# Kernel optimization log

Hardware: AMD Instinct MI355X
Metric: run time of the kernel (lower is better)

## Reference

```python
import jax, jax.numpy as jnp
import numpy as np

B, S, E, HD = 32, 1024, 768, 64
NUM_IMAGE_PATCHES = 49


def setup_inputs() -> dict:
    key = jax.random.key(0)
    ks = jax.random.split(key, 9)
    w = 0.02
    return {
        "decoder_sequence": jax.random.normal(ks[0], (B, S, E), dtype=jnp.float32),
        "Wq": jax.random.normal(ks[1], (E, HD), dtype=jnp.float32) * w,
        "bq": jnp.zeros((HD,), dtype=jnp.float32),
        "Wk": jax.random.normal(ks[2], (E, HD), dtype=jnp.float32) * w,
        "bk": jnp.zeros((HD,), dtype=jnp.float32),
        "Wv": jax.random.normal(ks[3], (E, HD), dtype=jnp.float32) * w,
        "bv": jnp.zeros((HD,), dtype=jnp.float32),
        "input_sequence_length": 975,
        "padding_mask": jax.random.randint(ks[4], (B, 1, S), 0, 2).astype(bool),
    }


def reference(decoder_sequence, Wq, bq, Wk, bk, Wv, bv, input_sequence_length, padding_mask):
    # single-head projections: [B,S,E] @ [E,HD] -> [B,S,HD]
    Q = decoder_sequence @ Wq + bq
    K = decoder_sequence @ Wk + bk
    V = decoder_sequence @ Wv + bv

    scores = jnp.einsum('bid,bjd->bij', Q, K) / jnp.sqrt(jnp.float32(HD))

    # mask: image-patch rows (i < 49) fully unmasked; text region is causal
    # (mask[49:,49:] = triu(-inf, diag=1)), i.e. -inf where i >= 49 and j > i.
    i = jnp.arange(S)[:, None]
    j = jnp.arange(S)[None, :]
    causal_bad = (i >= NUM_IMAGE_PATCHES) & (j > i)  # [S,S]
    scores = jnp.where(causal_bad[None, :, :], -jnp.inf, scores)

    # padding mask on keys, broadcast over queries: [B,1,S] -> [B,S,S]
    scores = jnp.where(padding_mask, -jnp.inf, scores)

    A = jax.nn.softmax(scores, axis=-1)
    H = jnp.einsum('bij,bjd->bid', A, V)
    return H
```

## Files before the change

### kernel.cpp

```cpp
#include <hip/hip_runtime.h>
#include <stdint.h>
#include <stddef.h>


typedef __attribute__((ext_vector_type(8))) short bf16x8;
typedef __attribute__((ext_vector_type(4))) float f32x4;

#define NIP 49
#define QSCALE 0.18033688011112042f

#define GLDS16(g, l)                                      \
  __builtin_amdgcn_global_load_lds(                       \
      (const __attribute__((address_space(1))) void*)(g), \
      (__attribute__((address_space(3))) void*)(l), 16, 0, 0)

__device__ __forceinline__ short f2b(float f) {
  union { float f; uint32_t u; } c; c.f = f;
  uint32_t u = c.u;
  uint32_t r = (u + 0x7fffu + ((u >> 16) & 1u)) >> 16;
  return (short)(uint16_t)r;
}

__global__ __launch_bounds__(256) void wt_kernel(
    const float* __restrict__ Wq, const float* __restrict__ Wk,
    const float* __restrict__ Wv, short* __restrict__ Wt) {
  int idx = blockIdx.x * 256 + threadIdx.x;
  int n = idx / 768;
  int k = idx - n * 768;
  const float* W = (n < 64) ? Wq : (n < 128) ? Wk : Wv;
  Wt[idx] = f2b(W[(size_t)k * 64 + (n & 63)]);
}

__global__ __launch_bounds__(256, 2) void proj_kernel(
    const float* __restrict__ X, const float* __restrict__ bq,
    const float* __restrict__ bk, const float* __restrict__ bv,
    const short* __restrict__ Wt, short* __restrict__ Qg,
    short* __restrict__ Kg, short* __restrict__ Vt) {
  __shared__ short lX[2][2][64][32];
  __shared__ short lW[2][2][192][32];
  const int tid = threadIdx.x;
  const int wid = tid >> 6, lane = tid & 63;
  const int l15 = lane & 15, q4 = lane >> 4;
  const int r0 = blockIdx.x * 64;

  float4 rx[4];
  auto xload = [&](int kb) {
#pragma unroll
    for (int i = 0; i < 4; ++i) {
      const int xi = tid + i * 256;
      rx[i] = *(const float4*)(X + (size_t)(r0 + (xi >> 4)) * 768 + kb + (xi & 15) * 4);
    }
  };
  auto xstage = [&](int buf) {
#pragma unroll
    for (int i = 0; i < 4; ++i) {
      const int xi = tid + i * 256;
      short4 s;
      s.x = f2b(rx[i].x); s.y = f2b(rx[i].y); s.z = f2b(rx[i].z); s.w = f2b(rx[i].w);
      *(short4*)&lX[buf][(xi & 15) >> 3][xi >> 4][(xi & 7) * 4] = s;
    }
  };
  const int wr = lane >> 2, wc = (lane & 3) * 8;
  auto wlds = [&](int buf, int kb) {
#pragma unroll
    for (int i = 0; i < 6; ++i) {
      const int fi = wid * 6 + i;
      const int j = fi >> 1, ks = fi & 1;
      GLDS16(Wt + (size_t)(j * 16 + wr) * 768 + kb + ks * 32 + wc,
             &lW[buf][ks][j * 16][0]);
    }
  };

  f32x4 acc[12];
#pragma unroll
  for (int c = 0; c < 12; ++c) acc[c] = (f32x4){0.f, 0.f, 0.f, 0.f};

  xload(0);
  wlds(0, 0);
  xstage(0);
  __syncthreads();

#pragma unroll
  for (int st = 0; st < 12; ++st) {
    const int cur = st & 1;
    if (st + 1 < 12) {
      xload((st + 1) * 64);
      wlds(cur ^ 1, (st + 1) * 64);
    }
#pragma unroll
    for (int ks = 0; ks < 2; ++ks) {
      bf16x8 a = *(const bf16x8*)&lX[cur][ks][wid * 16 + l15][q4 * 8];
#pragma unroll
      for (int c = 0; c < 12; ++c) {
        bf16x8 bw = *(const bf16x8*)&lW[cur][ks][c * 16 + l15][q4 * 8];
        acc[c] = __builtin_amdgcn_mfma_f32_16x16x32_bf16(a, bw, acc[c], 0, 0, 0);
      }
    }
    if (st + 1 < 12) xstage(cur ^ 1);
    __syncthreads();
  }

  const int b = r0 >> 10, s0 = r0 & 1023;
#pragma unroll
  for (int c = 0; c < 12; ++c) {
    const int mtx = c >> 2;
    const int h = (c & 3) * 16 + l15;
    if (mtx < 2) {
      const float bias = (mtx == 0 ? bq : bk)[h];
      short* op = (mtx == 0) ? Qg : Kg;
#pragma unroll
      for (int rr = 0; rr < 4; ++rr) {
        int row = r0 + wid * 16 + q4 * 4 + rr;
        float v = acc[c][rr] + bias;
        if (mtx == 0) v *= QSCALE;
        op[(size_t)row * 64 + h] = f2b(v);
      }
    } else {
      const float bias = bv[h];
      short4 sv;
      sv.x = f2b(acc[c][0] + bias); sv.y = f2b(acc[c][1] + bias);
      sv.z = f2b(acc[c][2] + bias); sv.w = f2b(acc[c][3] + bias);
      *(short4*)(Vt + ((size_t)(b * 64 + h) << 10) + s0 + wid * 16 + q4 * 4) = sv;
    }
  }
}

__global__ __launch_bounds__(256, 2) void attn_kernel(
    const short* __restrict__ Qg, const short* __restrict__ Kg,
    const short* __restrict__ Vt, const int* __restrict__ pad,
    float* __restrict__ out) {
  __shared__ short lK[2][2][128][32];
  __shared__ short lV[2][4][64][32];
  __shared__ short lP[4][16][68];
  __shared__ short lOnes[16][32];

  const int b = blockIdx.x;
  const int level = blockIdx.y;
  const int t = (level == 0) ? 0 : 16 - level;
  const int tid = threadIdx.x;
  const int wid = tid >> 6, lane = tid & 63;
  const int l15 = lane & 15, q4 = lane >> 4;
  const int qs = t * 64;
  const size_t base = (size_t)b * 1024;
  const int nkt = (t == 0) ? 8 : (t / 2 + 1);

  {
    int i0 = tid, i1 = tid + 256;
    ((short*)lOnes)[i0] = ((i0 >> 5) == 0) ? (short)0x3F80 : (short)0;
    if (i1 < 512) ((short*)lOnes)[i1] = ((i1 >> 5) == 0) ? (short)0x3F80 : (short)0;
  }

  const short* qrow = Qg + (base + qs + wid * 16 + l15) * 64;
  bf16x8 aq0 = *(const bf16x8*)(qrow + q4 * 8);
  bf16x8 aq1 = *(const bf16x8*)(qrow + 32 + q4 * 8);

  const int sr = lane >> 2, sc = (lane & 3) * 8;
  auto wlds_tile = [&](int buf, int kt) {
    const int kb = kt * 128;
#pragma unroll
    for (int i = 0; i < 4; ++i) {
      const int dh = i & 1, krow = wid * 32 + (i >> 1) * 16;
      GLDS16(Kg + (base + kb + krow + sr) * 64 + dh * 32 + sc,
             &lK[buf][dh][krow][0]);
    }
#pragma unroll
    for (int kq = 0; kq < 4; ++kq) {
      GLDS16(Vt + ((size_t)(b * 64 + wid * 16 + sr) << 10) + kb + kq * 32 + sc,
             &lV[buf][kq][wid * 16][0]);
    }
  };
  int pc[8];
  auto pload = [&](int kt) {
#pragma unroll
    for (int c = 0; c < 8; ++c) pc[c] = pad[base + kt * 128 + c * 16 + l15];
  };

  pload(0);
  wlds_tile(0, 0);
  __syncthreads();

  f32x4 o[5];
#pragma unroll
  for (int c = 0; c < 5; ++c) o[c] = (f32x4){0.f, 0.f, 0.f, 0.f};

  for (int kt = 0; kt < nkt; ++kt) {
    const int cur = kt & 1;
    const int kb = kt * 128;
    float padm[8];
#pragma unroll
    for (int c = 0; c < 8; ++c) padm[c] = (pc[c] != 0) ? 0.f : 1.f;
    if (kt + 1 < nkt) {
      wlds_tile(cur ^ 1, kt + 1);
      pload(kt + 1);
    }

    f32x4 s4[8];
#pragma unroll
    for (int c = 0; c < 8; ++c) {
      s4[c] = (f32x4){0.f, 0.f, 0.f, 0.f};
      bf16x8 b0 = *(const bf16x8*)&lK[cur][0][c * 16 + l15][q4 * 8];
      s4[c] = __builtin_amdgcn_mfma_f32_16x16x32_bf16(aq0, b0, s4[c], 0, 0, 0);
      bf16x8 b1 = *(const bf16x8*)&lK[cur][1][c * 16 + l15][q4 * 8];
      s4[c] = __builtin_amdgcn_mfma_f32_16x16x32_bf16(aq1, b1, s4[c], 0, 0, 0);
    }

    const bool diag = (t == 0) ? (kt == 0) : (kt == nkt - 1);
    const bool img = (t == 0 && kt > 0);
    float p[8][4];
#pragma unroll
    for (int rr = 0; rr < 4; ++rr) {
      const int qi = qs + wid * 16 + q4 * 4 + rr;
#pragma unroll
      for (int c = 0; c < 8; ++c) {
        float pv = exp2f(fminf(s4[c][rr], 80.f)) * padm[c];
        if (diag) {
          int j = kb + c * 16 + l15;
          if (qi >= NIP && j > qi) pv = 0.f;
        }
        if (img && qi >= NIP) pv = 0.f;
        p[c][rr] = pv;
      }
    }

#pragma unroll
    for (int half = 0; half < 2; ++half) {
#pragma unroll
      for (int rr = 0; rr < 4; ++rr)
#pragma unroll
        for (int c = 0; c < 4; ++c)
          lP[wid][q4 * 4 + rr][c * 16 + l15] = f2b(p[half * 4 + c][rr]);
      bf16x8 ap0 = *(const bf16x8*)&lP[wid][l15][q4 * 8];
      bf16x8 ap1 = *(const bf16x8*)&lP[wid][l15][32 + q4 * 8];
      const int kq0 = half * 2, kq1 = half * 2 + 1;
#pragma unroll
      for (int c = 0; c < 5; ++c) {
        bf16x8 b0 = (c < 4) ? *(const bf16x8*)&lV[cur][kq0][c * 16 + l15][q4 * 8]
                            : *(const bf16x8*)&lOnes[l15][q4 * 8];
        o[c] = __builtin_amdgcn_mfma_f32_16x16x32_bf16(ap0, b0, o[c], 0, 0, 0);
        bf16x8 b1 = (c < 4) ? *(const bf16x8*)&lV[cur][kq1][c * 16 + l15][q4 * 8]
                            : *(const bf16x8*)&lOnes[l15][q4 * 8];
        o[c] = __builtin_amdgcn_mfma_f32_16x16x32_bf16(ap1, b1, o[c], 0, 0, 0);
      }
    }
    __syncthreads();
  }

#pragma unroll
  for (int rr = 0; rr < 4; ++rr) {
    float l = __shfl(o[4][rr], lane & 48, 64);
    const float inv = (l > 0.f) ? 1.0f / l : 0.f;
    const size_t row = base + qs + wid * 16 + q4 * 4 + rr;
#pragma unroll
    for (int c = 0; c < 4; ++c)
      out[row * 64 + c * 16 + l15] = o[c][rr] * inv;
  }
}

extern "C" void kernel_launch(void* const* d_in, const int* in_sizes, int n_in,
                              void* d_out, int out_size, void* d_ws, size_t ws_size,
                              hipStream_t stream) {
  const float* X  = (const float*)d_in[0];
  const float* Wq = (const float*)d_in[1];
  const float* bq = (const float*)d_in[2];
  const float* Wk = (const float*)d_in[3];
  const float* bk = (const float*)d_in[4];
  const float* Wv = (const float*)d_in[5];
  const float* bv = (const float*)d_in[6];
  const int* pad  = (const int*)d_in[8];
  float* out = (float*)d_out;

  short* Qg = (short*)d_ws;
  short* Kg = Qg + 32768 * 64;
  short* Vt = Kg + 32768 * 64;
  short* Wt = Vt + 32768 * 64;

  wt_kernel<<<576, 256, 0, stream>>>(Wq, Wk, Wv, Wt);
  proj_kernel<<<512, 256, 0, stream>>>(X, bq, bk, bv, Wt, Qg, Kg, Vt);
  attn_kernel<<<dim3(32, 16), 256, 0, stream>>>(Qg, Kg, Vt, pad, out);
}
```

Before: 201.7 us.

## Drop LDS staging in projection GEMM, load operands directly from global

The projection kernel no longer double-buffers X and W tiles through shared memory with block barriers. Each wave now owns 16 rows, loads its X fragment straight into registers (prefetching one k-step ahead) and reads the W fragments directly from global/L2 for each MFMA. This removes the LDS traffic and __syncthreads overhead and raises the occupancy hint to 3 blocks per CU. In exchange, W is re-read from cache by every wave, global accesses are less coalesced, and the latency hiding now depends on occupancy.

Result: slower. 245.6 us (+21.8%).

```diff
diff --git a/kernel.cpp b/kernel.cpp
--- a/kernel.cpp
+++ b/kernel.cpp
@@ -31,73 +31,39 @@
   Wt[idx] = f2b(W[(size_t)k * 64 + (n & 63)]);
 }
 
-__global__ __launch_bounds__(256, 2) void proj_kernel(
+__global__ __launch_bounds__(256, 3) void proj_kernel(
     const float* __restrict__ X, const float* __restrict__ bq,
     const float* __restrict__ bk, const float* __restrict__ bv,
     const short* __restrict__ Wt, short* __restrict__ Qg,
     short* __restrict__ Kg, short* __restrict__ Vt) {
-  __shared__ short lX[2][2][64][32];
-  __shared__ short lW[2][2][192][32];
   const int tid = threadIdx.x;
   const int wid = tid >> 6, lane = tid & 63;
   const int l15 = lane & 15, q4 = lane >> 4;
-  const int r0 = blockIdx.x * 64;
-
-  float4 rx[4];
-  auto xload = [&](int kb) {
-#pragma unroll
-    for (int i = 0; i < 4; ++i) {
-      const int xi = tid + i * 256;
-      rx[i] = *(const float4*)(X + (size_t)(r0 + (xi >> 4)) * 768 + kb + (xi & 15) * 4);
-    }
-  };
-  auto xstage = [&](int buf) {
-#pragma unroll
-    for (int i = 0; i < 4; ++i) {
-      const int xi = tid + i * 256;
-      short4 s;
-      s.x = f2b(rx[i].x); s.y = f2b(rx[i].y); s.z = f2b(rx[i].z); s.w = f2b(rx[i].w);
-      *(short4*)&lX[buf][(xi & 15) >> 3][xi >> 4][(xi & 7) * 4] = s;
-    }
-  };
-  const int wr = lane >> 2, wc = (lane & 3) * 8;
-  auto wlds = [&](int buf, int kb) {
-#pragma unroll
-    for (int i = 0; i < 6; ++i) {
-      const int fi = wid * 6 + i;
-      const int j = fi >> 1, ks = fi & 1;
-      GLDS16(Wt + (size_t)(j * 16 + wr) * 768 + kb + ks * 32 + wc,
-             &lW[buf][ks][j * 16][0]);
-    }
-  };
+  const int r0 = (blockIdx.x * 4 + wid) * 16;
+
+  const float* xp = X + (size_t)(r0 + l15) * 768 + q4 * 8;
+  const short* wp = Wt + (size_t)l15 * 768 + q4 * 8;
 
   f32x4 acc[12];
 #pragma unroll
   for (int c = 0; c < 12; ++c) acc[c] = (f32x4){0.f, 0.f, 0.f, 0.f};
 
-  xload(0);
-  wlds(0, 0);
-  xstage(0);
-  __syncthreads();
-
-#pragma unroll
-  for (int st = 0; st < 12; ++st) {
-    const int cur = st & 1;
-    if (st + 1 < 12) {
-      xload((st + 1) * 64);
-      wlds(cur ^ 1, (st + 1) * 64);
-    }
-#pragma unroll
-    for (int ks = 0; ks < 2; ++ks) {
-      bf16x8 a = *(const bf16x8*)&lX[cur][ks][wid * 16 + l15][q4 * 8];
-#pragma unroll
-      for (int c = 0; c < 12; ++c) {
-        bf16x8 bw = *(const bf16x8*)&lW[cur][ks][c * 16 + l15][q4 * 8];
-        acc[c] = __builtin_amdgcn_mfma_f32_16x16x32_bf16(a, bw, acc[c], 0, 0, 0);
-      }
-    }
-    if (st + 1 < 12) xstage(cur ^ 1);
-    __syncthreads();
+  float4 a0 = *(const float4*)(xp);
+  float4 a1 = *(const float4*)(xp + 4);
+
+  for (int k0 = 0; k0 < 768; k0 += 32) {
+    bf16x8 a;
+    a[0] = f2b(a0.x); a[1] = f2b(a0.y); a[2] = f2b(a0.z); a[3] = f2b(a0.w);
+    a[4] = f2b(a1.x); a[5] = f2b(a1.y); a[6] = f2b(a1.z); a[7] = f2b(a1.w);
+    if (k0 + 32 < 768) {
+      a0 = *(const float4*)(xp + k0 + 32);
+      a1 = *(const float4*)(xp + k0 + 36);
+    }
+#pragma unroll
+    for (int c = 0; c < 12; ++c) {
+      bf16x8 bw = *(const bf16x8*)(wp + (size_t)c * 16 * 768 + k0);
+      acc[c] = __builtin_amdgcn_mfma_f32_16x16x32_bf16(a, bw, acc[c], 0, 0, 0);
+    }
   }
 
   const int b = r0 >> 10, s0 = r0 & 1023;
@@ -110,7 +76,7 @@
       short* op = (mtx == 0) ? Qg : Kg;
 #pragma unroll
       for (int rr = 0; rr < 4; ++rr) {
-        int row = r0 + wid * 16 + q4 * 4 + rr;
+        int row = r0 + q4 * 4 + rr;
         float v = acc[c][rr] + bias;
         if (mtx == 0) v *= QSCALE;
         op[(size_t)row * 64 + h] = f2b(v);
@@ -120,7 +86,7 @@
       short4 sv;
       sv.x = f2b(acc[c][0] + bias); sv.y = f2b(acc[c][1] + bias);
       sv.z = f2b(acc[c][2] + bias); sv.w = f2b(acc[c][3] + bias);
-      *(short4*)(Vt + ((size_t)(b * 64 + h) << 10) + s0 + wid * 16 + q4 * 4) = sv;
+      *(short4*)(Vt + ((size_t)(b * 64 + h) << 10) + s0 + q4 * 4) = sv;
     }
   }
 }
```
